# Kernel tuning notes

Hardware: AMD Instinct MI355X
Metric: run time of the kernel (lower is better)

Reference implementation:

```python
import jax, jax.numpy as jnp
import numpy as np

# ---- configuration matching init_kwargs ----
D_IN, D_HID, D_OUT = 4096, 4096, 4096
INTRINSIC = 1024            # size of trainable vector V
BATCH = 512
Q = float(min(np.log(60000.0) ** 2 / INTRINSIC, 1.0))  # fastJL_vars: q = min(ln(60000)^2/d, 1)

PARAM_SHAPES = {
    'W1': (D_HID, D_IN),   # nn.Linear weight is (out, in)
    'b1': (D_HID,),
    'W2': (D_OUT, D_HID),
    'b2': (D_OUT,),
}

def _next_pow2(n):
    return 1 << int(np.ceil(np.log2(n)))

def fwht(x):
    """Fast Walsh-Hadamard transform over a length-2^k vector.
    Mirrors fast_walsh_hadamard_torched: at step i, split axis i of the
    [2]*k view into halves a,b and concatenate (a+b, a-b)."""
    n = x.shape[0]
    steps = int(round(np.log2(n)))
    for i in range(steps):
        y = x.reshape(2 ** i, 2, -1)
        a, b = y[:, 0], y[:, 1]
        x = jnp.stack([a + b, a - b], axis=1).reshape(n)
    return x

def fastjl(V, D, PP, shape):
    """ret = (1/dd) * (PP * FWHT(D * pad(V, LL)))[:DD], reshaped to param shape."""
    LL = D.shape[0]
    dd = V.shape[0]
    DD = int(np.prod(shape))
    v_pad = jnp.zeros((LL,), V.dtype).at[:dd].set(V)
    h = fwht(D * v_pad)
    return ((PP * h)[:DD] / dd).reshape(shape)

def setup_inputs() -> dict:
    key = jax.random.key(0)
    ks = jax.random.split(key, 4 + 3 * len(PARAM_SHAPES) + len(PARAM_SHAPES))
    inp = {}
    inp['x'] = jax.random.normal(ks[0], (BATCH, D_IN), dtype=jnp.float32)
    inp['V'] = jax.random.normal(ks[1], (INTRINSIC,), dtype=jnp.float32) * 0.01
    i = 2
    for name, shape in PARAM_SHAPES.items():
        # initial (frozen) parameter values
        scale = 1.0 / np.sqrt(shape[-1]) if len(shape) > 1 else 0.0
        inp[name + '_init'] = jax.random.normal(ks[i], shape, dtype=jnp.float32) * scale
        LL = _next_pow2(int(np.prod(shape)))
        # D: Rademacher +-1
        rad = jax.random.bernoulli(ks[i + 1], 0.5, (LL,))
        inp['D_' + name] = jnp.where(rad, 1.0, -1.0).astype(jnp.float32)
        # PP = B * R, B ~ Bernoulli(1-q), R ~ N(0, (1/q)^2)
        B = jax.random.bernoulli(ks[i + 2], 1.0 - Q, (LL,)).astype(jnp.float32)
        R = jax.random.normal(ks[i + 3], (LL,), dtype=jnp.float32) * (1.0 / Q)
        inp['PP_' + name] = B * R
        i += 4
    return inp

def reference(x, V, W1_init, b1_init, W2_init, b2_init,
              D_W1, PP_W1, D_b1, PP_b1, D_W2, PP_W2, D_b2, PP_b2):
    # Reconstruct each wrapped-module parameter: init + FastJL(V)
    W1 = W1_init + fastjl(V, D_W1, PP_W1, PARAM_SHAPES['W1'])
    b1 = b1_init + fastjl(V, D_b1, PP_b1, PARAM_SHAPES['b1'])
    W2 = W2_init + fastjl(V, D_W2, PP_W2, PARAM_SHAPES['W2'])
    b2 = b2_init + fastjl(V, D_b2, PP_b2, PARAM_SHAPES['b2'])
    # wrapped module forward: Linear -> ReLU -> Linear
    h = jax.nn.relu(x @ W1.T + b1)
    return h @ W2.T + b2
```

## Files before the change

### kernel.cpp

```cpp
#include <hip/hip_runtime.h>
#include <hip/hip_bf16.h>
#include <stdint.h>

typedef unsigned short u16;
typedef __attribute__((ext_vector_type(8))) short short8;
typedef __attribute__((ext_vector_type(4))) float f32x4;

__device__ __forceinline__ u16 f2bf(float f) {
    union { float f; uint32_t u; } c; c.f = f;
    uint32_t u = c.u;
    u += 0x7fffu + ((u >> 16) & 1u);
    return (u16)(u >> 16);
}

__device__ __forceinline__ void glds16(const void* g, void* l) {
    __builtin_amdgcn_global_load_lds(
        (const __attribute__((address_space(1))) uint32_t*)g,
        (__attribute__((address_space(3))) uint32_t*)l,
        16, 0, 0);
}

__global__ void fwht_g_kernel(const float* __restrict__ V,
                              const float* __restrict__ D0, const float* __restrict__ D1,
                              const float* __restrict__ D2, const float* __restrict__ D3,
                              float* __restrict__ g) {
    __shared__ float s[1024];
    int t = threadIdx.x;
    const float* D = (blockIdx.x == 0) ? D0 : (blockIdx.x == 1) ? D1 :
                     (blockIdx.x == 2) ? D2 : D3;
    s[t] = D[t] * V[t];
    __syncthreads();
    #pragma unroll
    for (int st = 512; st >= 1; st >>= 1) {
        float a = s[t];
        float b = s[t ^ st];
        __syncthreads();
        s[t] = (t & st) ? (b - a) : (a + b);
        __syncthreads();
    }
    g[blockIdx.x * 1024 + t] = s[t] * (1.0f / 1024.0f);
}

__global__ void bias_kernel(const float* __restrict__ init, const float* __restrict__ PP,
                            const float* __restrict__ g, float* __restrict__ out, int n) {
    int i = blockIdx.x * blockDim.x + threadIdx.x;
    if (i < n) out[i] = init[i] + PP[i] * g[i & 1023];
}

__global__ void cast_kernel(const float* __restrict__ in, u16* __restrict__ out, int n4) {
    int i = blockIdx.x * blockDim.x + threadIdx.x;
    if (i >= n4) return;
    float4 v = ((const float4*)in)[i];
    uint32_t lo = (uint32_t)f2bf(v.x) | ((uint32_t)f2bf(v.y) << 16);
    uint32_t hi = (uint32_t)f2bf(v.z) | ((uint32_t)f2bf(v.w) << 16);
    ((uint2*)out)[i] = make_uint2(lo, hi);
}

__global__ __launch_bounds__(256, 2) void gemm_fused(const u16* __restrict__ A,
                                                     const float* __restrict__ Winit,
                                                     const float* __restrict__ PP,
                                                     const float* __restrict__ gvec,
                                                     float* __restrict__ P,
                                                     int M, int N, int K, int Kslice) {
    constexpr int BM = 256, BN = 64, BK = 64;
    __shared__ u16 As[BM * BK];
    __shared__ u16 Bs[BN * BK];

    const int t    = threadIdx.x;
    const int wid  = t >> 6;
    const int lane = t & 63;
    const int fr   = lane & 15;
    const int fq   = lane >> 4;

    const int bn = blockIdx.x, bm = blockIdx.y, sk = blockIdx.z;
    const int k_beg = sk * Kslice;
    const int nstep = Kslice / BK;

    const u16* Abase = A + (size_t)(bm * BM) * K;

    const int rB = t >> 4;
    const int cB = (t & 15) * 4;
    const float* Wb = Winit + (size_t)(bn * BN + rB) * K;
    const float* Pb = PP    + (size_t)(bn * BN + rB) * K;
    const size_t rstride = (size_t)16 * K;

    float4 wi0, wi1, wi2, wi3, pp0, pp1, pp2, pp3;

#define PREFETCH_W(k0) do {                                   \
        const float* wp_ = Wb + (k0) + cB;                    \
        const float* qp_ = Pb + (k0) + cB;                    \
        wi0 = *(const float4*)(wp_);                          \
        wi1 = *(const float4*)(wp_ + rstride);                \
        wi2 = *(const float4*)(wp_ + 2 * rstride);            \
        wi3 = *(const float4*)(wp_ + 3 * rstride);            \
        pp0 = *(const float4*)(qp_);                          \
        pp1 = *(const float4*)(qp_ + rstride);                \
        pp2 = *(const float4*)(qp_ + 2 * rstride);            \
        pp3 = *(const float4*)(qp_ + 3 * rstride);            \
    } while (0)

#define WRITE_B(k0) do {                                                          \
        float4 gv_ = *(const float4*)(gvec + (((k0) + cB) & 1023));               \
        uint32_t lo_, hi_;                                                        \
        lo_ = (uint32_t)f2bf(wi0.x + pp0.x * gv_.x) |                             \
              ((uint32_t)f2bf(wi0.y + pp0.y * gv_.y) << 16);                      \
        hi_ = (uint32_t)f2bf(wi0.z + pp0.z * gv_.z) |                             \
              ((uint32_t)f2bf(wi0.w + pp0.w * gv_.w) << 16);                      \
        *(uint2*)(Bs + (rB +  0) * BK + cB) = make_uint2(lo_, hi_);               \
        lo_ = (uint32_t)f2bf(wi1.x + pp1.x * gv_.x) |                             \
              ((uint32_t)f2bf(wi1.y + pp1.y * gv_.y) << 16);                      \
        hi_ = (uint32_t)f2bf(wi1.z + pp1.z * gv_.z) |                             \
              ((uint32_t)f2bf(wi1.w + pp1.w * gv_.w) << 16);                      \
        *(uint2*)(Bs + (rB + 16) * BK + cB) = make_uint2(lo_, hi_);               \
        lo_ = (uint32_t)f2bf(wi2.x + pp2.x * gv_.x) |                             \
              ((uint32_t)f2bf(wi2.y + pp2.y * gv_.y) << 16);                      \
        hi_ = (uint32_t)f2bf(wi2.z + pp2.z * gv_.z) |                             \
              ((uint32_t)f2bf(wi2.w + pp2.w * gv_.w) << 16);                      \
        *(uint2*)(Bs + (rB + 32) * BK + cB) = make_uint2(lo_, hi_);               \
        lo_ = (uint32_t)f2bf(wi3.x + pp3.x * gv_.x) |                             \
              ((uint32_t)f2bf(wi3.y + pp3.y * gv_.y) << 16);                      \
        hi_ = (uint32_t)f2bf(wi3.z + pp3.z * gv_.z) |                             \
              ((uint32_t)f2bf(wi3.w + pp3.w * gv_.w) << 16);                      \
        *(uint2*)(Bs + (rB + 48) * BK + cB) = make_uint2(lo_, hi_);               \
    } while (0)

#define STAGE_A(k0) do {                                                          \
        _Pragma("unroll")                                                         \
        for (int q_ = 0; q_ < 8; ++q_) {                                          \
            int L_ = q_ * 256 + t;                                                \
            int row_ = L_ >> 3;                                                   \
            int cg_ = (L_ & 7) * 8;                                               \
            glds16(Abase + (size_t)row_ * K + (k0) + cg_, As + L_ * 8);           \
        }                                                                         \
    } while (0)

    f32x4 acc[4][4];
    #pragma unroll
    for (int m = 0; m < 4; ++m)
        #pragma unroll
        for (int n = 0; n < 4; ++n)
            acc[m][n] = (f32x4){0.f, 0.f, 0.f, 0.f};

    PREFETCH_W(k_beg);
    STAGE_A(k_beg);
    WRITE_B(k_beg);
    __syncthreads();

    #pragma unroll 1
    for (int s = 0; s < nstep; ++s) {
        const int k0 = k_beg + s * BK;
        const bool nxt = (s + 1 < nstep);
        if (nxt) PREFETCH_W(k0 + BK);

        #pragma unroll
        for (int ks = 0; ks < 2; ++ks) {
            short8 a[4], b[4];
            #pragma unroll
            for (int m = 0; m < 4; ++m)
                a[m] = *(const short8*)(As + (wid * 64 + m * 16 + fr) * BK + ks * 32 + fq * 8);
            #pragma unroll
            for (int n = 0; n < 4; ++n)
                b[n] = *(const short8*)(Bs + (n * 16 + fr) * BK + ks * 32 + fq * 8);
            #pragma unroll
            for (int m = 0; m < 4; ++m)
                #pragma unroll
                for (int n = 0; n < 4; ++n)
                    acc[m][n] = __builtin_amdgcn_mfma_f32_16x16x32_bf16(a[m], b[n], acc[m][n], 0, 0, 0);
        }
        __syncthreads();
        if (nxt) {
            STAGE_A(k0 + BK);
            WRITE_B(k0 + BK);
        }
        __syncthreads();
    }

#undef PREFETCH_W
#undef WRITE_B
#undef STAGE_A

    float* Pp = P + (size_t)sk * M * N;
    #pragma unroll
    for (int m = 0; m < 4; ++m) {
        int grow0 = bm * BM + wid * 64 + m * 16 + fq * 4;
        #pragma unroll
        for (int n = 0; n < 4; ++n) {
            int gcol = bn * BN + n * 16 + fr;
            #pragma unroll
            for (int j = 0; j < 4; ++j)
                Pp[(size_t)(grow0 + j) * N + gcol] = acc[m][n][j];
        }
    }
}

template <typename OutT, bool RELU, int S>
__global__ void reduce_kernel(const float* __restrict__ P, const float* __restrict__ bias,
                              OutT* __restrict__ out, int MN, int N) {
    int i = blockIdx.x * blockDim.x + threadIdx.x;
    if (i * 4 >= MN) return;
    int e = i * 4;
    int col = e & (N - 1);
    float4 acc = ((const float4*)(P + e))[0];
    #pragma unroll
    for (int s = 1; s < S; ++s) {
        float4 p = ((const float4*)(P + (size_t)s * MN + e))[0];
        acc.x += p.x; acc.y += p.y; acc.z += p.z; acc.w += p.w;
    }
    float4 bv = *((const float4*)(bias + col));
    acc.x += bv.x; acc.y += bv.y; acc.z += bv.z; acc.w += bv.w;
    if (RELU) {
        acc.x = fmaxf(acc.x, 0.f); acc.y = fmaxf(acc.y, 0.f);
        acc.z = fmaxf(acc.z, 0.f); acc.w = fmaxf(acc.w, 0.f);
    }
    if constexpr (sizeof(OutT) == 2) {
        uint32_t lo = (uint32_t)f2bf(acc.x) | ((uint32_t)f2bf(acc.y) << 16);
        uint32_t hi = (uint32_t)f2bf(acc.z) | ((uint32_t)f2bf(acc.w) << 16);
        ((uint2*)out)[i] = make_uint2(lo, hi);
    } else {
        ((float4*)out)[i] = acc;
    }
}

extern "C" void kernel_launch(void* const* d_in, const int* in_sizes, int n_in,
                              void* d_out, int out_size, void* d_ws, size_t ws_size,
                              hipStream_t stream) {
    (void)in_sizes; (void)n_in; (void)out_size; (void)ws_size;

    const float* x       = (const float*)d_in[0];
    const float* V       = (const float*)d_in[1];
    const float* W1_init = (const float*)d_in[2];
    const float* D_W1    = (const float*)d_in[3];
    const float* PP_W1   = (const float*)d_in[4];
    const float* b1_init = (const float*)d_in[5];
    const float* D_b1    = (const float*)d_in[6];
    const float* PP_b1   = (const float*)d_in[7];
    const float* W2_init = (const float*)d_in[8];
    const float* D_W2    = (const float*)d_in[9];
    const float* PP_W2   = (const float*)d_in[10];
    const float* b2_init = (const float*)d_in[11];
    const float* D_b2    = (const float*)d_in[12];
    const float* PP_b2   = (const float*)d_in[13];

    constexpr size_t MB = 1024 * 1024;
    char* ws = (char*)d_ws;
    float* g    = (float*)(ws);
    float* b1w  = (float*)(ws + 16384);
    float* b2w  = (float*)(ws + 32768);
    u16*   xb   = (u16*)(ws + 65536);
    u16*   hb   = (u16*)(ws + 65536 + 4 * MB);
    float* Pbuf = (float*)(ws + 65536 + 8 * MB);

    const int M = 512, N = 4096, K = 4096, S = 4, Kslice = K / S;

    fwht_g_kernel<<<4, 1024, 0, stream>>>(V, D_W1, D_b1, D_W2, D_b2, g);
    bias_kernel<<<4, 1024, 0, stream>>>(b1_init, PP_b1, g + 1024, b1w, 4096);
    bias_kernel<<<4, 1024, 0, stream>>>(b2_init, PP_b2, g + 3072, b2w, 4096);
    cast_kernel<<<2048, 256, 0, stream>>>(x, xb, M * K / 4);

    gemm_fused<<<dim3(N / 64, M / 256, S), 256, 0, stream>>>(xb, W1_init, PP_W1, g, Pbuf, M, N, K, Kslice);
    reduce_kernel<u16, true, S><<<M * N / 4 / 256, 256, 0, stream>>>(Pbuf, b1w, hb, M * N, N);

    gemm_fused<<<dim3(N / 64, M / 256, S), 256, 0, stream>>>(hb, W2_init, PP_W2, g + 2048, Pbuf, M, N, K, Kslice);
    reduce_kernel<float, false, S><<<M * N / 4 / 256, 256, 0, stream>>>(Pbuf, b2w, (float*)d_out, M * N, N);
}
```

Measured before the change: 144.6 us.

## Double-buffer LDS tiles and prefetch weights two steps ahead in fused GEMM

```diff
diff --git a/kernel.cpp b/kernel.cpp
--- a/kernel.cpp
+++ b/kernel.cpp
@@ -6,11 +6,11 @@
 typedef __attribute__((ext_vector_type(8))) short short8;
 typedef __attribute__((ext_vector_type(4))) float f32x4;
 
-__device__ __forceinline__ u16 f2bf(float f) {
+__device__ __forceinline__ uint32_t f2bf(float f) {
     union { float f; uint32_t u; } c; c.f = f;
     uint32_t u = c.u;
     u += 0x7fffu + ((u >> 16) & 1u);
-    return (u16)(u >> 16);
+    return u >> 16;
 }
 
 __device__ __forceinline__ void glds16(const void* g, void* l) {
@@ -18,6 +18,12 @@
         (const __attribute__((address_space(1))) uint32_t*)g,
         (__attribute__((address_space(3))) uint32_t*)l,
         16, 0, 0);
+}
+
+__device__ __forceinline__ uint2 wrow2(float4 wi, float4 pp, float4 gv) {
+    uint32_t lo = f2bf(wi.x + pp.x * gv.x) | (f2bf(wi.y + pp.y * gv.y) << 16);
+    uint32_t hi = f2bf(wi.z + pp.z * gv.z) | (f2bf(wi.w + pp.w * gv.w) << 16);
+    return make_uint2(lo, hi);
 }
 
 __global__ void fwht_g_kernel(const float* __restrict__ V,
@@ -51,8 +57,8 @@
     int i = blockIdx.x * blockDim.x + threadIdx.x;
     if (i >= n4) return;
     float4 v = ((const float4*)in)[i];
-    uint32_t lo = (uint32_t)f2bf(v.x) | ((uint32_t)f2bf(v.y) << 16);
-    uint32_t hi = (uint32_t)f2bf(v.z) | ((uint32_t)f2bf(v.w) << 16);
+    uint32_t lo = f2bf(v.x) | (f2bf(v.y) << 16);
+    uint32_t hi = f2bf(v.z) | (f2bf(v.w) << 16);
     ((uint2*)out)[i] = make_uint2(lo, hi);
 }
 
@@ -63,8 +69,8 @@
                                                      float* __restrict__ P,
                                                      int M, int N, int K, int Kslice) {
     constexpr int BM = 256, BN = 64, BK = 64;
-    __shared__ u16 As[BM * BK];
-    __shared__ u16 Bs[BN * BK];
+    __shared__ u16 As[2][BM * BK];
+    __shared__ u16 Bs[2][BN * BK];
 
     const int t    = threadIdx.x;
     const int wid  = t >> 6;
@@ -74,7 +80,7 @@
 
     const int bn = blockIdx.x, bm = blockIdx.y, sk = blockIdx.z;
     const int k_beg = sk * Kslice;
-    const int nstep = Kslice / BK;
+    const int npair = (Kslice / BK) / 2;
 
     const u16* Abase = A + (size_t)(bm * BM) * K;
 
@@ -84,54 +90,82 @@
     const float* Pb = PP    + (size_t)(bn * BN + rB) * K;
     const size_t rstride = (size_t)16 * K;
 
-    float4 wi0, wi1, wi2, wi3, pp0, pp1, pp2, pp3;
-
-#define PREFETCH_W(k0) do {                                   \
+    float4 w00, w01, w02, w03, p00, p01, p02, p03;
+    float4 w10, w11, w12, w13, p10, p11, p12, p13;
+
+#define PF_W0(k0) do {                                        \
         const float* wp_ = Wb + (k0) + cB;                    \
         const float* qp_ = Pb + (k0) + cB;                    \
-        wi0 = *(const float4*)(wp_);                          \
-        wi1 = *(const float4*)(wp_ + rstride);                \
-        wi2 = *(const float4*)(wp_ + 2 * rstride);            \
-        wi3 = *(const float4*)(wp_ + 3 * rstride);            \
-        pp0 = *(const float4*)(qp_);                          \
-        pp1 = *(const float4*)(qp_ + rstride);                \
-        pp2 = *(const float4*)(qp_ + 2 * rstride);            \
-        pp3 = *(const float4*)(qp_ + 3 * rstride);            \
-    } while (0)
-
-#define WRITE_B(k0) do {                                                          \
+        w00 = *(const float4*)(wp_);                          \
+        w01 = *(const float4*)(wp_ + rstride);                \
+        w02 = *(const float4*)(wp_ + 2 * rstride);            \
+        w03 = *(const float4*)(wp_ + 3 * rstride);            \
+        p00 = *(const float4*)(qp_);                          \
+        p01 = *(const float4*)(qp_ + rstride);                \
+        p02 = *(const float4*)(qp_ + 2 * rstride);            \
+        p03 = *(const float4*)(qp_ + 3 * rstride);            \
+    } while (0)
+
+#define PF_W1(k0) do {                                        \
+        const float* wp_ = Wb + (k0) + cB;                    \
+        const float* qp_ = Pb + (k0) + cB;                    \
+        w10 = *(const float4*)(wp_);                          \
+        w11 = *(const float4*)(wp_ + rstride);                \
+        w12 = *(const float4*)(wp_ + 2 * rstride);            \
+        w13 = *(const float4*)(wp_ + 3 * rstride);            \
+        p10 = *(const float4*)(qp_);                          \
+        p11 = *(const float4*)(qp_ + rstride);                \
+        p12 = *(const float4*)(qp_ + 2 * rstride);            \
+        p13 = *(const float4*)(qp_ + 3 * rstride);            \
+    } while (0)
+
+#define WRITE_B0(k0, buf) do {                                                    \
         float4 gv_ = *(const float4*)(gvec + (((k0) + cB) & 1023));               \
-        uint32_t lo_, hi_;                                                        \
-        lo_ = (uint32_t)f2bf(wi0.x + pp0.x * gv_.x) |                             \
-              ((uint32_t)f2bf(wi0.y + pp0.y * gv_.y) << 16);                      \
-        hi_ = (uint32_t)f2bf(wi0.z + pp0.z * gv_.z) |                             \
-              ((uint32_t)f2bf(wi0.w + pp0.w * gv_.w) << 16);                      \
-        *(uint2*)(Bs + (rB +  0) * BK + cB) = make_uint2(lo_, hi_);               \
-        lo_ = (uint32_t)f2bf(wi1.x + pp1.x * gv_.x) |                             \
-              ((uint32_t)f2bf(wi1.y + pp1.y * gv_.y) << 16);                      \
-        hi_ = (uint32_t)f2bf(wi1.z + pp1.z * gv_.z) |                             \
-              ((uint32_t)f2bf(wi1.w + pp1.w * gv_.w) << 16);                      \
-        *(uint2*)(Bs + (rB + 16) * BK + cB) = make_uint2(lo_, hi_);               \
-        lo_ = (uint32_t)f2bf(wi2.x + pp2.x * gv_.x) |                             \
-              ((uint32_t)f2bf(wi2.y + pp2.y * gv_.y) << 16);                      \
-        hi_ = (uint32_t)f2bf(wi2.z + pp2.z * gv_.z) |                             \
-              ((uint32_t)f2bf(wi2.w + pp2.w * gv_.w) << 16);                      \
-        *(uint2*)(Bs + (rB + 32) * BK + cB) = make_uint2(lo_, hi_);               \
-        lo_ = (uint32_t)f2bf(wi3.x + pp3.x * gv_.x) |                             \
-              ((uint32_t)f2bf(wi3.y + pp3.y * gv_.y) << 16);                      \
-        hi_ = (uint32_t)f2bf(wi3.z + pp3.z * gv_.z) |                             \
-              ((uint32_t)f2bf(wi3.w + pp3.w * gv_.w) << 16);                      \
-        *(uint2*)(Bs + (rB + 48) * BK + cB) = make_uint2(lo_, hi_);               \
-    } while (0)
-
-#define STAGE_A(k0) do {                                                          \
+        *(uint2*)(Bs[buf] + (rB +  0) * BK + cB) = wrow2(w00, p00, gv_);          \
+        *(uint2*)(Bs[buf] + (rB + 16) * BK + cB) = wrow2(w01, p01, gv_);          \
+        *(uint2*)(Bs[buf] + (rB + 32) * BK + cB) = wrow2(w02, p02, gv_);          \
+        *(uint2*)(Bs[buf] + (rB + 48) * BK + cB) = wrow2(w03, p03, gv_);          \
+    } while (0)
+
+#define WRITE_B1(k0, buf) do {                                                    \
+        float4 gv_ = *(const float4*)(gvec + (((k0) + cB) & 1023));               \
+        *(uint2*)(Bs[buf] + (rB +  0) * BK + cB) = wrow2(w10, p10, gv_);          \
+        *(uint2*)(Bs[buf] + (rB + 16) * BK + cB) = wrow2(w11, p11, gv_);          \
+        *(uint2*)(Bs[buf] + (rB + 32) * BK + cB) = wrow2(w12, p12, gv_);          \
+        *(uint2*)(Bs[buf] + (rB + 48) * BK + cB) = wrow2(w13, p13, gv_);          \
+    } while (0)
+
+#define STAGE_A(k0, buf) do {                                                     \
         _Pragma("unroll")                                                         \
         for (int q_ = 0; q_ < 8; ++q_) {                                          \
             int L_ = q_ * 256 + t;                                                \
             int row_ = L_ >> 3;                                                   \
             int cg_ = (L_ & 7) * 8;                                               \
-            glds16(Abase + (size_t)row_ * K + (k0) + cg_, As + L_ * 8);           \
+            glds16(Abase + (size_t)row_ * K + (k0) + cg_, As[buf] + L_ * 8);      \
         }                                                                         \
+    } while (0)
+
+#define MFMA_STEP(buf) do {                                                       \
+        __builtin_amdgcn_s_setprio(1);                                            \
+        _Pragma("unroll")                                                         \
+        for (int ks_ = 0; ks_ < 2; ++ks_) {                                       \
+            short8 a_[4], b_[4];                                                  \
+            _Pragma("unroll")                                                     \
+            for (int m_ = 0; m_ < 4; ++m_)                                        \
+                a_[m_] = *(const short8*)(As[buf] +                               \
+                          (wid * 64 + m_ * 16 + fr) * BK + ks_ * 32 + fq * 8);    \
+            _Pragma("unroll")                                                     \
+            for (int n_ = 0; n_ < 4; ++n_)                                        \
+                b_[n_] = *(const short8*)(Bs[buf] +                               \
+                          (n_ * 16 + fr) * BK + ks_ * 32 + fq * 8);               \
+            _Pragma("unroll")                                                     \
+            for (int m_ = 0; m_ < 4; ++m_)                                        \
+                _Pragma("unroll")                                                 \
+                for (int n_ = 0; n_ < 4; ++n_)                                    \
+                    acc[m_][n_] = __builtin_amdgcn_mfma_f32_16x16x32_bf16(        \
+                        a_[m_], b_[n_], acc[m_][n_], 0, 0, 0);                    \
+        }                                                                         \
+        __builtin_amdgcn_s_setprio(0);                                            \
     } while (0)
 
     f32x4 acc[4][4];
@@ -141,43 +175,38 @@
         for (int n = 0; n < 4; ++n)
             acc[m][n] = (f32x4){0.f, 0.f, 0.f, 0.f};
 
-    PREFETCH_W(k_beg);
-    STAGE_A(k_beg);
-    WRITE_B(k_beg);
+    PF_W0(k_beg);
+    PF_W1(k_beg + BK);
+    STAGE_A(k_beg, 0);
+    WRITE_B0(k_beg, 0);
     __syncthreads();
 
+    int kk = k_beg;
     #pragma unroll 1
-    for (int s = 0; s < nstep; ++s) {
-        const int k0 = k_beg + s * BK;
-        const bool nxt = (s + 1 < nstep);
-        if (nxt) PREFETCH_W(k0 + BK);
-
-        #pragma unroll
-        for (int ks = 0; ks < 2; ++ks) {
-            short8 a[4], b[4];
-            #pragma unroll
-            for (int m = 0; m < 4; ++m)
-                a[m] = *(const short8*)(As + (wid * 64 + m * 16 + fr) * BK + ks * 32 + fq * 8);
-            #pragma unroll
-            for (int n = 0; n < 4; ++n)
-                b[n] = *(const short8*)(Bs + (n * 16 + fr) * BK + ks * 32 + fq * 8);
-            #pragma unroll
-            for (int m = 0; m < 4; ++m)
-                #pragma unroll
-                for (int n = 0; n < 4; ++n)
-                    acc[m][n] = __builtin_amdgcn_mfma_f32_16x16x32_bf16(a[m], b[n], acc[m][n], 0, 0, 0);
-        }
-        __syncthreads();
-        if (nxt) {
-            STAGE_A(k0 + BK);
-            WRITE_B(k0 + BK);
-        }
-        __syncthreads();
-    }
-
-#undef PREFETCH_W
-#undef WRITE_B
+    for (int p = 0; p < npair - 1; ++p, kk += 2 * BK) {
+        PF_W0(kk + 2 * BK);
+        STAGE_A(kk + BK, 1);
+        WRITE_B1(kk + BK, 1);
+        MFMA_STEP(0);
+        __syncthreads();
+        PF_W1(kk + 3 * BK);
+        STAGE_A(kk + 2 * BK, 0);
+        WRITE_B0(kk + 2 * BK, 0);
+        MFMA_STEP(1);
+        __syncthreads();
+    }
+    STAGE_A(kk + BK, 1);
+    WRITE_B1(kk + BK, 1);
+    MFMA_STEP(0);
+    __syncthreads();
+    MFMA_STEP(1);
+
+#undef PF_W0
+#undef PF_W1
+#undef WRITE_B0
+#undef WRITE_B1
 #undef STAGE_A
+#undef MFMA_STEP
 
     float* Pp = P + (size_t)sk * M * N;
     #pragma unroll
@@ -213,8 +242,8 @@
         acc.z = fmaxf(acc.z, 0.f); acc.w = fmaxf(acc.w, 0.f);
     }
     if constexpr (sizeof(OutT) == 2) {
-        uint32_t lo = (uint32_t)f2bf(acc.x) | ((uint32_t)f2bf(acc.y) << 16);
-        uint32_t hi = (uint32_t)f2bf(acc.z) | ((uint32_t)f2bf(acc.w) << 16);
+        uint32_t lo = f2bf(acc.x) | (f2bf(acc.y) << 16);
+        uint32_t hi = f2bf(acc.z) | (f2bf(acc.w) << 16);
         ((uint2*)out)[i] = make_uint2(lo, hi);
     } else {
         ((float4*)out)[i] = acc;
```

Measured after the change: 144.2 us. About the same (-0.3%).
